# Performance work log

Hardware: AMD Instinct MI355X
Metric: run time of the kernel (lower is better)

## Reference

```python
import jax, jax.numpy as jnp
import numpy as np

CHUNK_SIZE = 256


def setup_inputs() -> dict:
    key = jax.random.key(0)
    kq, kk, kv = jax.random.split(key, 3)
    b, h, L, d, dv = 2, 16, 4096, 16, 64
    return {
        "q": jax.random.normal(kq, (b, h, L, d), dtype=jnp.float32),
        "k": jax.random.normal(kk, (b, h, L, d), dtype=jnp.float32),
        "v": jax.random.normal(kv, (b, h, L, dv), dtype=jnp.float32),
    }


def reference(q, k, v):
    b, h, L, d = q.shape
    dv = v.shape[-1]
    cs = CHUNK_SIZE
    n = L // cs

    q = q * d ** (-0.5)

    # ---- normalizer z over full sequence ----
    k_cumsum = jnp.cumsum(k, axis=-2)                               # [b,h,L,d]
    kk_cumsum = jnp.cumsum(k[..., :, None] * k[..., None, :], axis=-3)  # [b,h,L,d,d]
    z = (q * k_cumsum).sum(-1)
    z = z + 0.5 * jnp.einsum('bhld,bhle,bhlde->bhl', q, q, kk_cumsum)
    z = z + (jnp.arange(L, dtype=z.dtype) + 1.0)[None, None, :]

    # ---- zeroth-order term ----
    o_const = jnp.cumsum(v, axis=-2)                                # [b,h,L,dv]

    # ---- chunked view ----
    qc = q.reshape(b, h, n, cs, d)
    kc = k.reshape(b, h, n, cs, d)
    vc = v.reshape(b, h, n, cs, dv)

    # intra-chunk quadratic attention: S + 0.5*S^2, causal-masked
    s = jnp.einsum('bhnqd,bhnkd->bhnqk', qc, kc)                    # [b,h,n,cs,cs]
    s = s + 0.5 * s ** 2
    causal_mask = jnp.tril(jnp.ones((cs, cs), dtype=bool))
    s = jnp.where(causal_mask, s, jnp.zeros((), dtype=s.dtype))
    o = jnp.einsum('bhnqk,bhnkf->bhnqf', s, vc)                     # [b,h,n,cs,dv]

    # inter-chunk quadratic state: cumulative K x K x V from previous chunks
    kv_quad = jnp.einsum('bhncd,bhnce,bhncf->bhndef', kc, kc, vc)   # [b,h,n,d,d,dv]
    kv_quad = jnp.cumsum(kv_quad, axis=2)
    kv_quad = jnp.concatenate(
        [jnp.zeros_like(kv_quad[:, :, :1]), kv_quad[:, :, :-1]], axis=2)
    o = o + 0.5 * jnp.einsum('bhndef,bhncd,bhnce->bhncf', kv_quad, qc, qc)

    # inter-chunk linear state: cumulative K x V from previous chunks
    kv_lin = jnp.einsum('bhncd,bhnce->bhnde', kc, vc)               # [b,h,n,d,dv]
    kv_lin = jnp.cumsum(kv_lin, axis=2)
    kv_lin = jnp.concatenate(
        [jnp.zeros_like(kv_lin[:, :, :1]), kv_lin[:, :, :-1]], axis=2)
    o = o + jnp.einsum('bhnde,bhncd->bhnce', kv_lin, qc)

    o = o.reshape(b, h, L, dv) + o_const
    return o / (z[..., None] + 1e-6)
```

## Files before the change

kernel.cpp:

```cpp
#include <hip/hip_runtime.h>
#include <cstddef>

#define BH    32
#define LSEQ  4096
#define D     16
#define DV    64
#define CS    256
#define NC    16
#define NF    160
#define NZ    65
#define KSTEPS 5

typedef short short8 __attribute__((ext_vector_type(8)));
typedef float f32x4 __attribute__((ext_vector_type(4)));

#define OFF_KBF 0u
#define OFF_VT  (4u*1024u*1024u)
#define OFF_ST  (OFF_VT + (unsigned)(BH*NZ*LSEQ*2))

__device__ __forceinline__ unsigned f2bf(float x) {
  unsigned u = __float_as_uint(x);
  return (u + 0x7FFFu + ((u >> 16) & 1u)) >> 16;
}
__device__ __forceinline__ short8 zero8() {
  short8 z = {0,0,0,0,0,0,0,0};
  return z;
}

__device__ __forceinline__ unsigned feat_tbl(int f) {
  if (f == 0)  return 16u | (16u << 8);
  if (f <= 16) return (unsigned)(f - 1) | (16u << 8);
  if (f < 137) {
    int p = f - 17, off = 0;
    for (int d = 0; d < 15; ++d) {
      int cnt = 15 - d;
      if (p < off + cnt) return (unsigned)d | ((unsigned)(d + 1 + p - off) << 8);
      off += cnt;
    }
  }
  if (f < 153) {
    int d = f - 137;
    return (unsigned)d | ((unsigned)d << 8) | (1u << 16);
  }
  return 17u | (17u << 8);
}

__global__ __launch_bounds__(320) void pass_a(const float* __restrict__ k,
                                              const float* __restrict__ v,
                                              unsigned* __restrict__ kbf_u32,
                                              unsigned* __restrict__ vt_u32,
                                              unsigned short* __restrict__ st) {
  __shared__ float kx[CS][18];
  __shared__ __align__(16) unsigned short vt_lds[NZ][264];
  __shared__ unsigned tbl[NF];
  int blk = blockIdx.x, bh = blk >> 4, c = blk & 15;
  int t = threadIdx.x, w = t >> 6, lane = t & 63, quad = lane >> 4, n16 = lane & 15;

  {
    const float2* kc2 = (const float2*)(k + ((size_t)bh * LSEQ + c * CS) * D);
    unsigned* kbd = kbf_u32 + ((size_t)bh * LSEQ + c * CS) * D / 2;
    for (int i = t; i < 2048; i += 320) {
      float2 v2 = kc2[i];
      kbd[i] = f2bf(v2.x) | (f2bf(v2.y) << 16);
      int j = i >> 3, dd = (i & 7) * 2;
      kx[j][dd] = v2.x; kx[j][dd + 1] = v2.y;
    }
    for (int i = t; i < CS; i += 320) { kx[i][16] = 1.f; kx[i][17] = 0.f; }
  }
  {
    const float* vb = v + ((size_t)bh * LSEQ + c * CS) * DV;
    for (int i = t; i < CS * DV; i += 320) {
      int j = i >> 6, f = i & 63;
      vt_lds[f][j] = (unsigned short)f2bf(vb[i]);
    }
    for (int i = t; i < CS; i += 320) vt_lds[64][i] = (unsigned short)0x3F80;
  }
  if (t < NF) tbl[t] = feat_tbl(t);
  __syncthreads();

  {
    unsigned* vtg = vt_u32 + (size_t)bh * NZ * (LSEQ / 2) + c * (CS / 2);
    for (int i = t; i < NZ * (CS / 2); i += 320) {
      int f = i >> 7, jp = (i & 127) * 2;
      vtg[(size_t)f * (LSEQ / 2) + (i & 127)] =
          (unsigned)vt_lds[f][jp] | ((unsigned)vt_lds[f][jp + 1] << 16);
    }
  }

  f32x4 acc[2][5];
#pragma unroll
  for (int mm = 0; mm < 2; ++mm)
#pragma unroll
    for (int nt = 0; nt < 5; ++nt) acc[mm][nt] = (f32x4){0.f, 0.f, 0.f, 0.f};

  for (int jt = 0; jt < 8; ++jt) {
    short8 afr[2];
#pragma unroll
    for (int mm = 0; mm < 2; ++mm) {
      int feat = (w * 2 + mm) * 16 + n16;
      unsigned tv = tbl[feat];
      int d = tv & 255, e = (tv >> 8) & 255;
      short8 a;
#pragma unroll
      for (int i = 0; i < 8; ++i) {
        int jj = jt * 32 + quad * 8 + i;
        a[i] = (short)f2bf(kx[jj][d] * kx[jj][e]);
      }
      afr[mm] = a;
    }
#pragma unroll
    for (int nt = 0; nt < 5; ++nt) {
      int ncol = nt * 16 + n16;
      short8 b = zero8();
      if (ncol < NZ) b = *(const short8*)(&vt_lds[ncol][jt * 32 + quad * 8]);
      acc[0][nt] = __builtin_amdgcn_mfma_f32_16x16x32_bf16(afr[0], b, acc[0][nt], 0, 0, 0);
      acc[1][nt] = __builtin_amdgcn_mfma_f32_16x16x32_bf16(afr[1], b, acc[1][nt], 0, 0, 0);
    }
  }

  unsigned short* stc = st + (size_t)(bh * NC + c) * NZ * NF;
#pragma unroll
  for (int mm = 0; mm < 2; ++mm)
#pragma unroll
    for (int nt = 0; nt < 5; ++nt) {
      int col = nt * 16 + n16;
      if (col < NZ) {
        unsigned lo = f2bf(acc[mm][nt][0]) | (f2bf(acc[mm][nt][1]) << 16);
        unsigned hi = f2bf(acc[mm][nt][2]) | (f2bf(acc[mm][nt][3]) << 16);
        int feat0 = (w * 2 + mm) * 16 + quad * 4;
        *(uint2*)(stc + (size_t)col * NF + feat0) = make_uint2(lo, hi);
      }
    }
}

__global__ __launch_bounds__(256) void pass_b(unsigned short* __restrict__ st) {
  const int PER = NZ * NF;
  const int TOT = BH * PER;
  int idx = blockIdx.x * 256 + threadIdx.x;
  if (idx >= TOT) return;
  int bh = idx / PER, r = idx - bh * PER;
  unsigned short* p = st + (size_t)bh * NC * PER + r;
  float run = 0.f;
#pragma unroll
  for (int c = 0; c < NC; ++c) {
    unsigned short uv = p[(size_t)c * PER];
    float val = __uint_as_float(((unsigned)uv) << 16);
    p[(size_t)c * PER] = (unsigned short)f2bf(run);
    run += val;
  }
}

__global__ __launch_bounds__(512) void pass_c(const float* __restrict__ q,
                                              const unsigned short* __restrict__ kbf,
                                              const unsigned short* __restrict__ vt,
                                              const unsigned short* __restrict__ st,
                                              float* __restrict__ out) {
  __shared__ float qx[CS][18];
  __shared__ unsigned tbl[NF];
  __shared__ __align__(16) unsigned short ptile[8][32 * 40];
  __shared__ float zline[CS];
  int blk = blockIdx.x, bh = blk >> 4, c = blk & 15;
  const size_t base = (size_t)bh * LSEQ + (size_t)c * CS;
  const float* qc = q + base * D;
  int t = threadIdx.x, w = t >> 6, lane = t & 63, quad = lane >> 4, n16 = lane & 15;

  for (int i = t; i < CS * D; i += 512) {
    int row = i >> 4, dd = i & 15;
    qx[row][dd] = qc[i] * 0.25f;
  }
  for (int i = t; i < CS; i += 512) { qx[i][16] = 1.f; qx[i][17] = 0.f; }
  if (t < NF) tbl[t] = feat_tbl(t);
  __syncthreads();

  f32x4 acc[2][5];
#pragma unroll
  for (int mm = 0; mm < 2; ++mm)
#pragma unroll
    for (int nt = 0; nt < 5; ++nt) acc[mm][nt] = (f32x4){0.f, 0.f, 0.f, 0.f};

  if (c > 0) {
    const unsigned short* stc = st + (size_t)(bh * NC + c) * NZ * NF;
    for (int ks = 0; ks < KSTEPS; ++ks) {
      short8 afr[2];
#pragma unroll
      for (int mm = 0; mm < 2; ++mm) {
        const float* qrow = qx[(w * 2 + mm) * 16 + n16];
        short8 a;
#pragma unroll
        for (int i = 0; i < 8; ++i) {
          int f = ks * 32 + quad * 8 + i;
          unsigned tv = tbl[f];
          float val = qrow[tv & 255] * qrow[(tv >> 8) & 255];
          if (tv & 0x10000u) val *= 0.5f;
          a[i] = (short)f2bf(val);
        }
        afr[mm] = a;
      }
#pragma unroll
      for (int nt = 0; nt < 5; ++nt) {
        int ncol = nt * 16 + n16;
        short8 b = zero8();
        if (ncol < NZ) b = *(const short8*)(stc + (size_t)ncol * NF + ks * 32 + quad * 8);
        acc[0][nt] = __builtin_amdgcn_mfma_f32_16x16x32_bf16(afr[0], b, acc[0][nt], 0, 0, 0);
        acc[1][nt] = __builtin_amdgcn_mfma_f32_16x16x32_bf16(afr[1], b, acc[1][nt], 0, 0, 0);
      }
    }
  }

  short8 qfr[2];
#pragma unroll
  for (int mm = 0; mm < 2; ++mm) {
    int m = (w * 2 + mm) * 16 + n16;
    short8 a = zero8();
    if (quad < 2) {
#pragma unroll
      for (int i = 0; i < 8; ++i) a[i] = (short)f2bf(qx[m][quad * 8 + i]);
    }
    qfr[mm] = a;
  }
  const unsigned short* kbc = kbf + base * D;
  const unsigned short* vtb = vt + (size_t)bh * NZ * LSEQ + (size_t)c * CS;
  unsigned short* pw = &ptile[w][0];
  short8 ones;
#pragma unroll
  for (int i = 0; i < 8; ++i) ones[i] = (short)0x3F80;

  for (int jt = 0; jt <= w; ++jt) {
    short8 kb[2];
#pragma unroll
    for (int ntk = 0; ntk < 2; ++ntk) {
      short8 b = zero8();
      if (quad < 2)
        b = *(const short8*)(kbc + (size_t)(jt * 32 + ntk * 16 + n16) * D + quad * 8);
      kb[ntk] = b;
    }
    f32x4 zf = (f32x4){0.f, 0.f, 0.f, 0.f};
    f32x4 s[2][2];
#pragma unroll
    for (int mm = 0; mm < 2; ++mm)
#pragma unroll
      for (int ntk = 0; ntk < 2; ++ntk)
        s[mm][ntk] = __builtin_amdgcn_mfma_f32_16x16x32_bf16(qfr[mm], kb[ntk], zf, 0, 0, 0);
    bool diag = (jt == w);
#pragma unroll
    for (int mm = 0; mm < 2; ++mm)
#pragma unroll
      for (int ntk = 0; ntk < 2; ++ntk)
#pragma unroll
        for (int r = 0; r < 4; ++r) {
          float sv = s[mm][ntk][r];
          float phi = fmaf(0.5f * sv, sv, sv) + 1.0f;
          if (diag) {
            int qrow = mm * 16 + quad * 4 + r;
            int kcol = ntk * 16 + n16;
            if (kcol > qrow) phi = 0.f;
          }
          pw[(mm * 16 + quad * 4 + r) * 40 + ntk * 16 + n16] = (unsigned short)f2bf(phi);
        }
    short8 pa[2];
#pragma unroll
    for (int mm = 0; mm < 2; ++mm)
      pa[mm] = *(const short8*)(pw + (mm * 16 + n16) * 40 + quad * 8);
#pragma unroll
    for (int nt = 0; nt < 5; ++nt) {
      int ncol = nt * 16 + n16;
      short8 b;
      if (ncol < 64)       b = *(const short8*)(vtb + (size_t)ncol * LSEQ + jt * 32 + quad * 8);
      else if (ncol == 64) b = ones;
      else                 b = zero8();
      acc[0][nt] = __builtin_amdgcn_mfma_f32_16x16x32_bf16(pa[0], b, acc[0][nt], 0, 0, 0);
      acc[1][nt] = __builtin_amdgcn_mfma_f32_16x16x32_bf16(pa[1], b, acc[1][nt], 0, 0, 0);
    }
  }

  if (n16 == 0) {
#pragma unroll
    for (int mm = 0; mm < 2; ++mm)
#pragma unroll
      for (int r = 0; r < 4; ++r)
        zline[(w * 2 + mm) * 16 + quad * 4 + r] = acc[mm][4][r];
  }
  float* oc = out + base * DV;
#pragma unroll
  for (int mm = 0; mm < 2; ++mm)
#pragma unroll
    for (int r = 0; r < 4; ++r) {
      int qrow = (w * 2 + mm) * 16 + quad * 4 + r;
      float inv = 1.0f / (zline[qrow] + 1e-6f);
#pragma unroll
      for (int nt = 0; nt < 4; ++nt)
        oc[(size_t)qrow * DV + nt * 16 + n16] = acc[mm][nt][r] * inv;
    }
}

extern "C" void kernel_launch(void* const* d_in, const int* in_sizes, int n_in,
                              void* d_out, int out_size, void* d_ws, size_t ws_size,
                              hipStream_t stream) {
  (void)in_sizes; (void)n_in; (void)out_size; (void)ws_size;
  const float* q = (const float*)d_in[0];
  const float* k = (const float*)d_in[1];
  const float* v = (const float*)d_in[2];
  char* wsb = (char*)d_ws;
  unsigned*       kbf32 = (unsigned*)(wsb + OFF_KBF);
  unsigned short* kbf   = (unsigned short*)(wsb + OFF_KBF);
  unsigned short* vtp   = (unsigned short*)(wsb + OFF_VT);
  unsigned short* stp   = (unsigned short*)(wsb + OFF_ST);

  pass_a<<<BH * NC, 320, 0, stream>>>(k, v, kbf32, (unsigned*)vtp, stp);
  pass_b<<<1300, 256, 0, stream>>>(stp);
  pass_c<<<BH * NC, 512, 0, stream>>>(q, kbf, vtp, stp, (float*)d_out);
}
```

Measured before the change: 134.8 us.

## Fuse three passes into one cooperative kernel with grid sync and per-block prefix sum

Merges the state-building, prefix-scan and output passes into a single cooperative kernel separated by a grid-wide barrier, removing two kernel launches and the global round trip of the scanned state. Each block now computes its own exclusive prefix over earlier chunks' states directly into LDS instead of relying on a separate scan kernel, which adds redundant reads (up to 15 chunks per block) but lets the inter-chunk MFMA read B from LDS. The old three-kernel path remains as a fallback if occupancy is insufficient for 512 co-resident blocks. A grid sync adds its own barrier cost.

```diff
diff --git a/kernel.cpp b/kernel.cpp
--- a/kernel.cpp
+++ b/kernel.cpp
@@ -1,4 +1,5 @@
 #include <hip/hip_runtime.h>
+#include <hip/hip_cooperative_groups.h>
 #include <cstddef>
 
 #define BH    32
@@ -10,6 +11,7 @@
 #define NF    160
 #define NZ    65
 #define KSTEPS 5
+#define PER   (NZ * NF)
 
 typedef short short8 __attribute__((ext_vector_type(8)));
 typedef float f32x4 __attribute__((ext_vector_type(4)));
@@ -21,6 +23,9 @@
 __device__ __forceinline__ unsigned f2bf(float x) {
   unsigned u = __float_as_uint(x);
   return (u + 0x7FFFu + ((u >> 16) & 1u)) >> 16;
+}
+__device__ __forceinline__ float bf2f(unsigned short u) {
+  return __uint_as_float(((unsigned)u) << 16);
 }
 __device__ __forceinline__ short8 zero8() {
   short8 z = {0,0,0,0,0,0,0,0};
@@ -43,6 +48,244 @@
     return (unsigned)d | ((unsigned)d << 8) | (1u << 16);
   }
   return 17u | (17u << 8);
+}
+
+struct SmemA {
+  float kx[CS][18];
+  __align__(16) unsigned short vt[NZ][264];
+};
+struct SmemC {
+  float qx[CS][18];
+  __align__(16) unsigned short st[NZ][168];
+  __align__(16) unsigned short ptile[8][1280];
+  float zline[CS];
+};
+union SmemU { SmemA a; SmemC c; };
+
+__global__ __launch_bounds__(512, 4) void unified(const float* __restrict__ q,
+                                                  const float* __restrict__ k,
+                                                  const float* __restrict__ v,
+                                                  unsigned* __restrict__ kbf_u32,
+                                                  unsigned* __restrict__ vt_u32,
+                                                  unsigned short* __restrict__ st,
+                                                  float* __restrict__ out) {
+  __shared__ SmemU sm;
+  __shared__ unsigned tbl[NF];
+  int blk = blockIdx.x, bh = blk >> 4, c = blk & 15;
+  int t = threadIdx.x, w = t >> 6, lane = t & 63, quad = lane >> 4, n16 = lane & 15;
+  const size_t base = (size_t)bh * LSEQ + (size_t)c * CS;
+
+  {
+    const float2* kc2 = (const float2*)(k + base * D);
+    unsigned* kbd = kbf_u32 + base * D / 2;
+    for (int i = t; i < 2048; i += 512) {
+      float2 v2 = kc2[i];
+      kbd[i] = f2bf(v2.x) | (f2bf(v2.y) << 16);
+      int j = i >> 3, dd = (i & 7) * 2;
+      sm.a.kx[j][dd] = v2.x; sm.a.kx[j][dd + 1] = v2.y;
+    }
+    for (int i = t; i < CS; i += 512) { sm.a.kx[i][16] = 1.f; sm.a.kx[i][17] = 0.f; }
+    const float* vb = v + base * DV;
+    for (int i = t; i < CS * DV; i += 512) {
+      int j = i >> 6, f = i & 63;
+      sm.a.vt[f][j] = (unsigned short)f2bf(vb[i]);
+    }
+    for (int i = t; i < CS; i += 512) sm.a.vt[64][i] = (unsigned short)0x3F80;
+    if (t < NF) tbl[t] = feat_tbl(t);
+  }
+  __syncthreads();
+  {
+    unsigned* vtg = vt_u32 + (size_t)bh * NZ * (LSEQ / 2) + c * (CS / 2);
+    for (int i = t; i < NZ * (CS / 2); i += 512) {
+      int f = i >> 7, jp = (i & 127) * 2;
+      vtg[(size_t)f * (LSEQ / 2) + (i & 127)] =
+          (unsigned)sm.a.vt[f][jp] | ((unsigned)sm.a.vt[f][jp + 1] << 16);
+    }
+  }
+  if (w < 5) {
+    f32x4 acc[2][5];
+#pragma unroll
+    for (int mm = 0; mm < 2; ++mm)
+#pragma unroll
+      for (int nt = 0; nt < 5; ++nt) acc[mm][nt] = (f32x4){0.f, 0.f, 0.f, 0.f};
+    for (int jt = 0; jt < 8; ++jt) {
+      short8 afr[2];
+#pragma unroll
+      for (int mm = 0; mm < 2; ++mm) {
+        int feat = (w * 2 + mm) * 16 + n16;
+        unsigned tv = tbl[feat];
+        int d = tv & 255, e = (tv >> 8) & 255;
+        short8 a;
+#pragma unroll
+        for (int i = 0; i < 8; ++i) {
+          int jj = jt * 32 + quad * 8 + i;
+          a[i] = (short)f2bf(sm.a.kx[jj][d] * sm.a.kx[jj][e]);
+        }
+        afr[mm] = a;
+      }
+#pragma unroll
+      for (int nt = 0; nt < 5; ++nt) {
+        int ncol = nt * 16 + n16;
+        short8 b = zero8();
+        if (ncol < NZ) b = *(const short8*)(&sm.a.vt[ncol][jt * 32 + quad * 8]);
+        acc[0][nt] = __builtin_amdgcn_mfma_f32_16x16x32_bf16(afr[0], b, acc[0][nt], 0, 0, 0);
+        acc[1][nt] = __builtin_amdgcn_mfma_f32_16x16x32_bf16(afr[1], b, acc[1][nt], 0, 0, 0);
+      }
+    }
+    unsigned short* stc = st + (size_t)(bh * NC + c) * PER;
+#pragma unroll
+    for (int mm = 0; mm < 2; ++mm)
+#pragma unroll
+      for (int nt = 0; nt < 5; ++nt) {
+        int col = nt * 16 + n16;
+        if (col < NZ) {
+          unsigned lo = f2bf(acc[mm][nt][0]) | (f2bf(acc[mm][nt][1]) << 16);
+          unsigned hi = f2bf(acc[mm][nt][2]) | (f2bf(acc[mm][nt][3]) << 16);
+          int feat0 = (w * 2 + mm) * 16 + quad * 4;
+          *(uint2*)(stc + (size_t)col * NF + feat0) = make_uint2(lo, hi);
+        }
+      }
+  }
+
+  cooperative_groups::this_grid().sync();
+
+  {
+    const float* qc = q + base * D;
+    for (int i = t; i < CS * D; i += 512) {
+      int row = i >> 4, dd = i & 15;
+      sm.c.qx[row][dd] = qc[i] * 0.25f;
+    }
+    for (int i = t; i < CS; i += 512) { sm.c.qx[i][16] = 1.f; sm.c.qx[i][17] = 0.f; }
+    if (c > 0) {
+      const unsigned short* stg = st + (size_t)bh * NC * PER;
+      for (int i = t; i < PER; i += 512) {
+        float s = 0.f;
+        for (int cc = 0; cc < c; ++cc) s += bf2f(stg[(size_t)cc * PER + i]);
+        int col = i / NF, ft = i - col * NF;
+        sm.c.st[col][ft] = (unsigned short)f2bf(s);
+      }
+    }
+  }
+  __syncthreads();
+
+  f32x4 acc[2][5];
+#pragma unroll
+  for (int mm = 0; mm < 2; ++mm)
+#pragma unroll
+    for (int nt = 0; nt < 5; ++nt) acc[mm][nt] = (f32x4){0.f, 0.f, 0.f, 0.f};
+
+  if (c > 0) {
+    for (int ks = 0; ks < KSTEPS; ++ks) {
+      short8 afr[2];
+#pragma unroll
+      for (int mm = 0; mm < 2; ++mm) {
+        const float* qrow = sm.c.qx[(w * 2 + mm) * 16 + n16];
+        short8 a;
+#pragma unroll
+        for (int i = 0; i < 8; ++i) {
+          int f = ks * 32 + quad * 8 + i;
+          unsigned tv = tbl[f];
+          float val = qrow[tv & 255] * qrow[(tv >> 8) & 255];
+          if (tv & 0x10000u) val *= 0.5f;
+          a[i] = (short)f2bf(val);
+        }
+        afr[mm] = a;
+      }
+#pragma unroll
+      for (int nt = 0; nt < 5; ++nt) {
+        int ncol = nt * 16 + n16;
+        short8 b = zero8();
+        if (ncol < NZ) b = *(const short8*)(&sm.c.st[ncol][ks * 32 + quad * 8]);
+        acc[0][nt] = __builtin_amdgcn_mfma_f32_16x16x32_bf16(afr[0], b, acc[0][nt], 0, 0, 0);
+        acc[1][nt] = __builtin_amdgcn_mfma_f32_16x16x32_bf16(afr[1], b, acc[1][nt], 0, 0, 0);
+      }
+    }
+  }
+
+  short8 qfr[2];
+#pragma unroll
+  for (int mm = 0; mm < 2; ++mm) {
+    int m = (w * 2 + mm) * 16 + n16;
+    short8 a = zero8();
+    if (quad < 2) {
+#pragma unroll
+      for (int i = 0; i < 8; ++i) a[i] = (short)f2bf(sm.c.qx[m][quad * 8 + i]);
+    }
+    qfr[mm] = a;
+  }
+  const unsigned short* kbc = (const unsigned short*)kbf_u32 + base * D;
+  const unsigned short* vtb = (const unsigned short*)vt_u32 + (size_t)bh * NZ * LSEQ + (size_t)c * CS;
+  unsigned short* pw = &sm.c.ptile[w][0];
+  short8 ones;
+#pragma unroll
+  for (int i = 0; i < 8; ++i) ones[i] = (short)0x3F80;
+
+  for (int jt = 0; jt <= w; ++jt) {
+    short8 kb[2];
+#pragma unroll
+    for (int ntk = 0; ntk < 2; ++ntk) {
+      short8 b = zero8();
+      if (quad < 2)
+        b = *(const short8*)(kbc + (size_t)(jt * 32 + ntk * 16 + n16) * D + quad * 8);
+      kb[ntk] = b;
+    }
+    f32x4 zf = (f32x4){0.f, 0.f, 0.f, 0.f};
+    f32x4 s[2][2];
+#pragma unroll
+    for (int mm = 0; mm < 2; ++mm)
+#pragma unroll
+      for (int ntk = 0; ntk < 2; ++ntk)
+        s[mm][ntk] = __builtin_amdgcn_mfma_f32_16x16x32_bf16(qfr[mm], kb[ntk], zf, 0, 0, 0);
+    bool diag = (jt == w);
+#pragma unroll
+    for (int mm = 0; mm < 2; ++mm)
+#pragma unroll
+      for (int ntk = 0; ntk < 2; ++ntk)
+#pragma unroll
+        for (int r = 0; r < 4; ++r) {
+          float sv = s[mm][ntk][r];
+          float phi = fmaf(0.5f * sv, sv, sv) + 1.0f;
+          if (diag) {
+            int qrow = mm * 16 + quad * 4 + r;
+            int kcol = ntk * 16 + n16;
+            if (kcol > qrow) phi = 0.f;
+          }
+          pw[(mm * 16 + quad * 4 + r) * 40 + ntk * 16 + n16] = (unsigned short)f2bf(phi);
+        }
+    short8 pa[2];
+#pragma unroll
+    for (int mm = 0; mm < 2; ++mm)
+      pa[mm] = *(const short8*)(pw + (mm * 16 + n16) * 40 + quad * 8);
+#pragma unroll
+    for (int nt = 0; nt < 5; ++nt) {
+      int ncol = nt * 16 + n16;
+      short8 b;
+      if (ncol < 64)       b = *(const short8*)(vtb + (size_t)ncol * LSEQ + jt * 32 + quad * 8);
+      else if (ncol == 64) b = ones;
+      else                 b = zero8();
+      acc[0][nt] = __builtin_amdgcn_mfma_f32_16x16x32_bf16(pa[0], b, acc[0][nt], 0, 0, 0);
+      acc[1][nt] = __builtin_amdgcn_mfma_f32_16x16x32_bf16(pa[1], b, acc[1][nt], 0, 0, 0);
+    }
+  }
+
+  if (n16 == 0) {
+#pragma unroll
+    for (int mm = 0; mm < 2; ++mm)
+#pragma unroll
+      for (int r = 0; r < 4; ++r)
+        sm.c.zline[(w * 2 + mm) * 16 + quad * 4 + r] = acc[mm][4][r];
+  }
+  float* oc = out + base * DV;
+#pragma unroll
+  for (int mm = 0; mm < 2; ++mm)
+#pragma unroll
+    for (int r = 0; r < 4; ++r) {
+      int qrow = (w * 2 + mm) * 16 + quad * 4 + r;
+      float inv = 1.0f / (sm.c.zline[qrow] + 1e-6f);
+#pragma unroll
+      for (int nt = 0; nt < 4; ++nt)
+        oc[(size_t)qrow * DV + nt * 16 + n16] = acc[mm][nt][r] * inv;
+    }
 }
 
 __global__ __launch_bounds__(320) void pass_a(const float* __restrict__ k,
@@ -55,7 +298,6 @@
   __shared__ unsigned tbl[NF];
   int blk = blockIdx.x, bh = blk >> 4, c = blk & 15;
   int t = threadIdx.x, w = t >> 6, lane = t & 63, quad = lane >> 4, n16 = lane & 15;
-
   {
     const float2* kc2 = (const float2*)(k + ((size_t)bh * LSEQ + c * CS) * D);
     unsigned* kbd = kbf_u32 + ((size_t)bh * LSEQ + c * CS) * D / 2;
@@ -77,7 +319,6 @@
   }
   if (t < NF) tbl[t] = feat_tbl(t);
   __syncthreads();
-
   {
     unsigned* vtg = vt_u32 + (size_t)bh * NZ * (LSEQ / 2) + c * (CS / 2);
     for (int i = t; i < NZ * (CS / 2); i += 320) {
@@ -86,13 +327,11 @@
           (unsigned)vt_lds[f][jp] | ((unsigned)vt_lds[f][jp + 1] << 16);
     }
   }
-
   f32x4 acc[2][5];
 #pragma unroll
   for (int mm = 0; mm < 2; ++mm)
 #pragma unroll
     for (int nt = 0; nt < 5; ++nt) acc[mm][nt] = (f32x4){0.f, 0.f, 0.f, 0.f};
-
   for (int jt = 0; jt < 8; ++jt) {
     short8 afr[2];
 #pragma unroll
@@ -117,8 +356,7 @@
       acc[1][nt] = __builtin_amdgcn_mfma_f32_16x16x32_bf16(afr[1], b, acc[1][nt], 0, 0, 0);
     }
   }
-
-  unsigned short* stc = st + (size_t)(bh * NC + c) * NZ * NF;
+  unsigned short* stc = st + (size_t)(bh * NC + c) * PER;
 #pragma unroll
   for (int mm = 0; mm < 2; ++mm)
 #pragma unroll
@@ -134,7 +372,6 @@
 }
 
 __global__ __launch_bounds__(256) void pass_b(unsigned short* __restrict__ st) {
-  const int PER = NZ * NF;
   const int TOT = BH * PER;
   int idx = blockIdx.x * 256 + threadIdx.x;
   if (idx >= TOT) return;
@@ -144,7 +381,7 @@
 #pragma unroll
   for (int c = 0; c < NC; ++c) {
     unsigned short uv = p[(size_t)c * PER];
-    float val = __uint_as_float(((unsigned)uv) << 16);
+    float val = bf2f(uv);
     p[(size_t)c * PER] = (unsigned short)f2bf(run);
     run += val;
   }
@@ -163,7 +400,6 @@
   const size_t base = (size_t)bh * LSEQ + (size_t)c * CS;
   const float* qc = q + base * D;
   int t = threadIdx.x, w = t >> 6, lane = t & 63, quad = lane >> 4, n16 = lane & 15;
-
   for (int i = t; i < CS * D; i += 512) {
     int row = i >> 4, dd = i & 15;
     qx[row][dd] = qc[i] * 0.25f;
@@ -171,15 +407,13 @@
   for (int i = t; i < CS; i += 512) { qx[i][16] = 1.f; qx[i][17] = 0.f; }
   if (t < NF) tbl[t] = feat_tbl(t);
   __syncthreads();
-
   f32x4 acc[2][5];
 #pragma unroll
   for (int mm = 0; mm < 2; ++mm)
 #pragma unroll
     for (int nt = 0; nt < 5; ++nt) acc[mm][nt] = (f32x4){0.f, 0.f, 0.f, 0.f};
-
   if (c > 0) {
-    const unsigned short* stc = st + (size_t)(bh * NC + c) * NZ * NF;
+    const unsigned short* stc = st + (size_t)(bh * NC + c) * PER;
     for (int ks = 0; ks < KSTEPS; ++ks) {
       short8 afr[2];
 #pragma unroll
@@ -206,7 +440,6 @@
       }
     }
   }
-
   short8 qfr[2];
 #pragma unroll
   for (int mm = 0; mm < 2; ++mm) {
@@ -224,7 +457,6 @@
   short8 ones;
 #pragma unroll
   for (int i = 0; i < 8; ++i) ones[i] = (short)0x3F80;
-
   for (int jt = 0; jt <= w; ++jt) {
     short8 kb[2];
 #pragma unroll
@@ -272,7 +504,6 @@
       acc[1][nt] = __builtin_amdgcn_mfma_f32_16x16x32_bf16(pa[1], b, acc[1][nt], 0, 0, 0);
     }
   }
-
   if (n16 == 0) {
 #pragma unroll
     for (int mm = 0; mm < 2; ++mm)
@@ -300,13 +531,25 @@
   const float* q = (const float*)d_in[0];
   const float* k = (const float*)d_in[1];
   const float* v = (const float*)d_in[2];
+  float* out = (float*)d_out;
   char* wsb = (char*)d_ws;
   unsigned*       kbf32 = (unsigned*)(wsb + OFF_KBF);
   unsigned short* kbf   = (unsigned short*)(wsb + OFF_KBF);
+  unsigned*       vt32  = (unsigned*)(wsb + OFF_VT);
   unsigned short* vtp   = (unsigned short*)(wsb + OFF_VT);
   unsigned short* stp   = (unsigned short*)(wsb + OFF_ST);
 
-  pass_a<<<BH * NC, 320, 0, stream>>>(k, v, kbf32, (unsigned*)vtp, stp);
-  pass_b<<<1300, 256, 0, stream>>>(stp);
-  pass_c<<<BH * NC, 512, 0, stream>>>(q, kbf, vtp, stp, (float*)d_out);
-}
+  int nb = 0;
+  hipError_t oe = hipOccupancyMaxActiveBlocksPerMultiprocessor(
+      &nb, reinterpret_cast<const void*>(unified), 512, 0);
+  if (oe == hipSuccess && nb >= 2) {
+    void* args[] = {(void*)&q, (void*)&k, (void*)&v,
+                    (void*)&kbf32, (void*)&vt32, (void*)&stp, (void*)&out};
+    hipLaunchCooperativeKernel(reinterpret_cast<const void*>(unified),
+                               dim3(BH * NC), dim3(512), args, 0, stream);
+  } else {
+    pass_a<<<BH * NC, 320, 0, stream>>>(k, v, kbf32, vt32, stp);
+    pass_b<<<1300, 256, 0, stream>>>(stp);
+    pass_c<<<BH * NC, 512, 0, stream>>>(q, kbf, vtp, stp, out);
+  }
+}
```

Result: no change. 134.4 us (-0.2%).
